# Optimization experiments

Measured on AMD Instinct MI355X. Metric: run time of the kernel, lower is better.

## Reference

```python
import jax, jax.numpy as jnp
import numpy as np

B, G, A, C = 128, 16, 8732, 21
THR = 0.5        # overlap_threshold
NEG_POS = 3      # neg_pos_ratio
VAR0, VAR1 = 0.1, 0.2  # loc_variance


def center_to_point(b):
    cxcy, wh = b[:, :2], b[:, 2:]
    return jnp.concatenate([cxcy - wh / 2, cxcy + wh / 2], axis=-1)


def iou_matrix(a, b):
    # a: [G,4], b: [A,4] point coords (x1,y1,x2,y2) -> [G,A]
    tl = jnp.maximum(a[:, None, :2], b[None, :, :2])
    br = jnp.minimum(a[:, None, 2:], b[None, :, 2:])
    wh = jnp.clip(br - tl, 0.0)
    inter = wh[..., 0] * wh[..., 1]
    area_a = (a[:, 2] - a[:, 0]) * (a[:, 3] - a[:, 1])
    area_b = (b[:, 2] - b[:, 0]) * (b[:, 3] - b[:, 1])
    return inter / (area_a[:, None] + area_b[None, :] - inter)


def encode(anchors, gt_pt):
    # anchors [A,4] (cx,cy,w,h); gt_pt [A,4] point coords
    g_cxcy = (gt_pt[:, :2] + gt_pt[:, 2:]) / 2
    g_wh = gt_pt[:, 2:] - gt_pt[:, :2]
    d_cxcy = (g_cxcy - anchors[:, :2]) / (anchors[:, 2:] * VAR0)
    d_wh = jnp.log(g_wh / anchors[:, 2:]) / VAR1
    return jnp.concatenate([d_cxcy, d_wh], axis=-1)


def match(boxes, labels, anchors, anchors_pt):
    # boxes [G,4] point coords, labels [G] int
    iou = iou_matrix(boxes, anchors_pt)           # [G,A]
    anchor_index = jnp.argmax(iou, axis=1)        # best anchor per gt, [G]
    gt_overlap = jnp.max(iou, axis=0)             # best gt overlap per anchor, [A]
    gt_index = jnp.argmax(iou, axis=0)            # best gt per anchor, [A]
    gt_overlap = gt_overlap.at[anchor_index].set(1.0)
    for i in range(G):
        gt_index = gt_index.at[anchor_index[i]].set(i)
    gt_coords = boxes[gt_index]                   # [A,4]
    loc = encode(anchors, gt_coords)              # [A,4]
    conf = labels[gt_index] + 1                   # [A], 0 reserved for background
    conf = jnp.where(gt_overlap < THR, 0, conf)
    return loc, conf


def setup_inputs() -> dict:
    key = jax.random.key(0)
    k1, k2, k3, k4, k5, k6, k7 = jax.random.split(key, 7)
    predict_offset_coords = jax.random.normal(k1, (B, A, 4), jnp.float32)
    predict_confidences = jax.random.normal(k2, (B, A, C), jnp.float32)
    # valid gt boxes: centers in [0.2,0.8], sizes in [0.05,0.3]
    c = jax.random.uniform(k3, (B, G, 2)) * 0.6 + 0.2
    s = jax.random.uniform(k4, (B, G, 2)) * 0.25 + 0.05
    target_boxes = jnp.concatenate([c - s / 2, c + s / 2], axis=-1)
    target_labels = jax.random.randint(k5, (B, G), 0, C - 1).astype(jnp.int32)
    # anchors in center-coord form (cx,cy,w,h), strictly positive w,h
    acx = jax.random.uniform(k6, (A, 2)) * 0.9 + 0.05
    awh = jax.random.uniform(k7, (A, 2)) * 0.25 + 0.05
    anchors = jnp.concatenate([acx, awh], axis=-1)
    return {"predict_offset_coords": predict_offset_coords,
            "predict_confidences": predict_confidences,
            "target_boxes": target_boxes,
            "target_labels": target_labels,
            "anchors": anchors}


def reference(predict_offset_coords, predict_confidences, target_boxes, target_labels, anchors):
    anchors_pt = center_to_point(anchors)
    loc_t, conf_t = jax.vmap(match, in_axes=(0, 0, None, None))(
        target_boxes, target_labels, anchors, anchors_pt)
    # labels are built without grad in the original (fresh tensors)
    loc_t = jax.lax.stop_gradient(loc_t)
    conf_t = jax.lax.stop_gradient(conf_t)

    is_pos = conf_t > 0                            # [B,A]
    # smooth L1 (beta=1), summed over positive anchors
    diff = predict_offset_coords - loc_t
    ad = jnp.abs(diff)
    sl1 = jnp.where(ad < 1.0, 0.5 * diff * diff, ad - 0.5)
    loss_loc = jnp.sum(sl1 * is_pos[..., None])

    num_pos = jnp.sum(is_pos, axis=1, keepdims=True)      # [B,1]
    n_total = jnp.sum(num_pos).astype(jnp.float32)
    num_neg = jnp.minimum(NEG_POS * num_pos, A - 1)        # [B,1]

    logp = jax.nn.log_softmax(predict_confidences, axis=-1)
    nll = -jnp.take_along_axis(logp, conf_t[..., None], axis=-1)[..., 0]  # [B,A]

    # hard-negative mining via double argsort
    aux = jnp.where(is_pos, 0.0, nll)
    order = jnp.argsort(-aux, axis=1)
    rank = jnp.argsort(order, axis=1)
    is_neg = rank < num_neg

    sel = jnp.logical_or(is_pos, is_neg)
    loss_cls = jnp.sum(jnp.where(sel, nll, 0.0))
    return loss_loc / n_total, loss_cls / n_total
```

## Files before the change

### kernel.cpp

```cpp
#include <hip/hip_runtime.h>
#include <math.h>

#define B_ 128
#define G_ 16
#define A_ 8732
#define C_ 21
#define THR_ 0.5f
#define NEG_POS_ 3
#define VAR0_ 0.1f
#define VAR1_ 0.2f

#define CHUNK_  512
#define NCHUNK_ ((A_ + CHUNK_ - 1) / CHUNK_)
#define TAILA_  (A_ - (NCHUNK_ - 1) * CHUNK_)
#define FULLV_  (CHUNK_ * C_ / 4)
#define TAILV_  (TAILA_ * C_ / 4)
#define NPT_    NCHUNK_

__global__ __launch_bounds__(512) void k_fused(
    const float* __restrict__ pred_off,
    const float* __restrict__ pred_conf,
    const float* __restrict__ tboxes,
    const int*   __restrict__ tlabels,
    const float* __restrict__ anchors,
    float*       __restrict__ lloc_b,
    float*       __restrict__ lcls_b,
    int*         __restrict__ npos_b)
{
    const int b    = blockIdx.x;
    const int tid  = threadIdx.x;
    const int lane = tid & 63;
    const int w    = tid >> 6;

    __shared__ float         s_ov[A_];
    __shared__ unsigned char s_gi[A_];
    __shared__ float         s_aux[A_];
    __shared__ float4        s_stage[FULLV_];
    __shared__ float s_boxlds[G_ * 4];
    __shared__ int   s_lab[G_];
    __shared__ unsigned long long s_gb[8 * G_];
    __shared__ int   s_forced[G_];
    __shared__ int   s_cnt[8];
    __shared__ int   s_c[2][8];
    __shared__ float s_r0[8], s_r1[8], s_r3[8];
    __shared__ int   s_r2[8];

    if (tid < G_ * 4) s_boxlds[tid] = tboxes[b * G_ * 4 + tid];
    if (tid < G_)     s_lab[tid]    = tlabels[b * G_ + tid];
    __syncthreads();

    float bx0[G_], by0[G_], bx1[G_], by1[G_], bar[G_];
    #pragma unroll
    for (int g = 0; g < G_; ++g) {
        bx0[g] = s_boxlds[g * 4 + 0];
        by0[g] = s_boxlds[g * 4 + 1];
        bx1[g] = s_boxlds[g * 4 + 2];
        by1[g] = s_boxlds[g * 4 + 3];
        bar[g] = (bx1[g] - bx0[g]) * (by1[g] - by0[g]);
    }

    unsigned long long gb[G_];
    #pragma unroll
    for (int g = 0; g < G_; ++g) gb[g] = 0ull;

    for (int a = tid; a < A_; a += 512) {
        float4 an = ((const float4*)anchors)[a];
        float ax0 = an.x - an.z * 0.5f, ay0 = an.y - an.w * 0.5f;
        float ax1 = an.x + an.z * 0.5f, ay1 = an.y + an.w * 0.5f;
        float area_b = (ax1 - ax0) * (ay1 - ay0);
        float bov = -1.f; int bg = 0;
        #pragma unroll
        for (int g = 0; g < G_; ++g) {
            float tlx = fmaxf(bx0[g], ax0);
            float tly = fmaxf(by0[g], ay0);
            float brx = fminf(bx1[g], ax1);
            float bry = fminf(by1[g], ay1);
            float wdt = fmaxf(brx - tlx, 0.f);
            float hgt = fmaxf(bry - tly, 0.f);
            float inter = wdt * hgt;
            float iou = inter / (bar[g] + area_b - inter);
            if (iou > bov) { bov = iou; bg = g; }
            unsigned long long pk =
                ((unsigned long long)__float_as_uint(iou) << 32) |
                (unsigned)(~(unsigned)a);
            if (pk > gb[g]) gb[g] = pk;
        }
        s_ov[a] = bov;
        s_gi[a] = (unsigned char)bg;
    }

    #pragma unroll
    for (int g = 0; g < G_; ++g) {
        #pragma unroll
        for (int off = 32; off > 0; off >>= 1) {
            unsigned long long o = __shfl_down(gb[g], off);
            if (o > gb[g]) gb[g] = o;
        }
    }
    if (lane == 0) {
        #pragma unroll
        for (int g = 0; g < G_; ++g) s_gb[w * G_ + g] = gb[g];
    }
    __syncthreads();
    if (tid < G_) {
        unsigned long long m = 0ull;
        #pragma unroll
        for (int wv = 0; wv < 8; ++wv) {
            unsigned long long v = s_gb[wv * G_ + tid];
            if (v > m) m = v;
        }
        s_forced[tid] = (int)(~(unsigned)(m & 0xFFFFFFFFull));
    }
    __syncthreads();
    if (tid == 0) {
        for (int g = 0; g < G_; ++g) {
            int a = s_forced[g];
            s_ov[a] = 1.0f;
            s_gi[a] = (unsigned char)g;
        }
    }

    float lloc = 0.f, pnll = 0.f;
    int   cnt  = 0;

    for (int cc = 0; cc < NCHUNK_; ++cc) {
        const int nv = (cc == NCHUNK_ - 1) ? TAILV_ : FULLV_;
        __syncthreads();
        const float4* g4 = (const float4*)pred_conf
                         + ((((size_t)b * A_) + (size_t)cc * CHUNK_) * C_ >> 2);
        for (int idx = tid; idx < nv; idx += 512) s_stage[idx] = g4[idx];
        __syncthreads();

        const int a = cc * CHUNK_ + tid;
        float auxv = 0.f;
        if (a < A_) {
            const float* sc = (const float*)s_stage + tid * C_;
            float m = sc[0];
            #pragma unroll
            for (int c = 1; c < C_; ++c) m = fmaxf(m, sc[c]);
            float s = 0.f;
            #pragma unroll
            for (int c = 0; c < C_; ++c) s += __expf(sc[c] - m);
            float lse = m + __logf(s);

            float ov  = s_ov[a];
            int   g   = s_gi[a];
            int  conf = (ov < THR_) ? 0 : (s_lab[g] + 1);
            float xc  = sc[conf];
            float nll = lse - xc;
            bool  pos = conf > 0;
            auxv = pos ? 0.f : nll;

            if (pos) {
                cnt++;
                pnll += nll;
                float4 an = ((const float4*)anchors)[a];
                float bxx0 = s_boxlds[g * 4 + 0], bxy0 = s_boxlds[g * 4 + 1];
                float bxx1 = s_boxlds[g * 4 + 2], bxy1 = s_boxlds[g * 4 + 3];
                float gcx = (bxx0 + bxx1) * 0.5f, gcy = (bxy0 + bxy1) * 0.5f;
                float gw = bxx1 - bxx0, gh = bxy1 - bxy0;
                float l0 = (gcx - an.x) / (an.z * VAR0_);
                float l1 = (gcy - an.y) / (an.w * VAR0_);
                float l2 = logf(gw / an.z) / VAR1_;
                float l3 = logf(gh / an.w) / VAR1_;
                float4 p = ((const float4*)pred_off)[(size_t)b * A_ + a];
                float d, ad;
                d = p.x - l0; ad = fabsf(d); lloc += (ad < 1.f) ? 0.5f * d * d : ad - 0.5f;
                d = p.y - l1; ad = fabsf(d); lloc += (ad < 1.f) ? 0.5f * d * d : ad - 0.5f;
                d = p.z - l2; ad = fabsf(d); lloc += (ad < 1.f) ? 0.5f * d * d : ad - 0.5f;
                d = p.w - l3; ad = fabsf(d); lloc += (ad < 1.f) ? 0.5f * d * d : ad - 0.5f;
            }
        }
        if (a < A_) s_aux[a] = auxv;
    }

    {
        int c = cnt;
        #pragma unroll
        for (int off = 32; off > 0; off >>= 1) c += __shfl_down(c, off);
        if (lane == 0) s_cnt[w] = c;
    }
    __syncthreads();
    int npos = 0;
    #pragma unroll
    for (int wv = 0; wv < 8; ++wv) npos += s_cnt[wv];
    if (tid == 0) npos_b[b] = npos;
    const int K = min(NEG_POS_ * npos, A_ - 1);

    unsigned u[NPT_];
    #pragma unroll
    for (int j = 0; j < NPT_; ++j) {
        int a = tid + j * 512;
        u[j] = (a < A_) ? __float_as_uint(s_aux[a]) : 0u;
    }

    unsigned lo = 0u, hi = 0x7f800000u;
    int it = 0;
    while (lo < hi) {
        unsigned mid = (lo + hi) >> 1;
        int c = 0;
        #pragma unroll
        for (int j = 0; j < NPT_; ++j) c += (u[j] > mid);
        #pragma unroll
        for (int off = 32; off > 0; off >>= 1) c += __shfl_down(c, off);
        if (lane == 0) s_c[it & 1][w] = c;
        __syncthreads();
        int total = 0;
        #pragma unroll
        for (int wv = 0; wv < 8; ++wv) total += s_c[it & 1][wv];
        if (total >= K) lo = mid + 1; else hi = mid;
        ++it;
    }

    int selc = 0; float selsm = 0.f;
    #pragma unroll
    for (int j = 0; j < NPT_; ++j) {
        if (u[j] > lo) { selc++; selsm += __uint_as_float(u[j]); }
    }

    #pragma unroll
    for (int off = 32; off > 0; off >>= 1) {
        lloc  += __shfl_down(lloc, off);
        pnll  += __shfl_down(pnll, off);
        selc  += __shfl_down(selc, off);
        selsm += __shfl_down(selsm, off);
    }
    if (lane == 0) { s_r0[w] = lloc; s_r1[w] = pnll; s_r2[w] = selc; s_r3[w] = selsm; }
    __syncthreads();
    if (tid == 0) {
        float L = 0.f, P = 0.f, S = 0.f; int Cc = 0;
        #pragma unroll
        for (int wv = 0; wv < 8; ++wv) {
            L += s_r0[wv]; P += s_r1[wv]; Cc += s_r2[wv]; S += s_r3[wv];
        }
        float T = __uint_as_float(lo);
        lloc_b[b] = L;
        lcls_b[b] = P + S + (float)(K - Cc) * T;
    }
}

__global__ __launch_bounds__(128) void k_fin(
    const float* __restrict__ lloc_b,
    const float* __restrict__ lcls_b,
    const int*   __restrict__ npos_b,
    float*       __restrict__ out)
{
    const int tid  = threadIdx.x;
    const int lane = tid & 63;
    const int w    = tid >> 6;
    __shared__ float s_l[2], s_c[2];
    __shared__ int   s_n[2];

    float L = lloc_b[tid];
    float Cc = lcls_b[tid];
    int   n = npos_b[tid];
    #pragma unroll
    for (int off = 32; off > 0; off >>= 1) {
        L  += __shfl_down(L, off);
        Cc += __shfl_down(Cc, off);
        n  += __shfl_down(n, off);
    }
    if (lane == 0) { s_l[w] = L; s_c[w] = Cc; s_n[w] = n; }
    __syncthreads();
    if (tid == 0) {
        float ntot = (float)(s_n[0] + s_n[1]);
        out[0] = (s_l[0] + s_l[1]) / ntot;
        out[1] = (s_c[0] + s_c[1]) / ntot;
    }
}

extern "C" void kernel_launch(void* const* d_in, const int* in_sizes, int n_in,
                              void* d_out, int out_size, void* d_ws, size_t ws_size,
                              hipStream_t stream) {
    const float* pred_off  = (const float*)d_in[0];
    const float* pred_conf = (const float*)d_in[1];
    const float* tboxes    = (const float*)d_in[2];
    const int*   tlabels   = (const int*)  d_in[3];
    const float* anchors   = (const float*)d_in[4];
    float* out = (float*)d_out;

    char* ws = (char*)d_ws;
    float* lloc_ws = (float*)ws;  ws += (size_t)B_ * sizeof(float);
    float* lcls_ws = (float*)ws;  ws += (size_t)B_ * sizeof(float);
    int*   npos_ws = (int*)ws;

    k_fused<<<B_, 512, 0, stream>>>(pred_off, pred_conf, tboxes, tlabels, anchors,
                                    lloc_ws, lcls_ws, npos_ws);
    k_fin<<<1, 128, 0, stream>>>(lloc_ws, lcls_ws, npos_ws, out);
}
```

Before: 265.8 us.

## Split matching into separate kernel and double-buffer conf staging via async LDS loads

Splits the fused kernel into a matching kernel that writes packed conf/gt-index per anchor plus positive counts, and a loss/selection kernel. The loss kernel double-buffers pred_conf chunks in LDS using global_load_lds direct-to-LDS loads, prefetching the next chunk while the current one is computed. This aims to hide global load latency and cut LDS pressure, which may raise occupancy. The cost is an extra kernel launch and a B*A int round-trip through global memory, with only 128 blocks.

```diff
diff --git a/kernel.cpp b/kernel.cpp
--- a/kernel.cpp
+++ b/kernel.cpp
@@ -10,6 +10,7 @@
 #define VAR0_ 0.1f
 #define VAR1_ 0.2f
 
+#define BA_     (B_ * A_)
 #define CHUNK_  512
 #define NCHUNK_ ((A_ + CHUNK_ - 1) / CHUNK_)
 #define TAILA_  (A_ - (NCHUNK_ - 1) * CHUNK_)
@@ -17,15 +18,19 @@
 #define TAILV_  (TAILA_ * C_ / 4)
 #define NPT_    NCHUNK_
 
-__global__ __launch_bounds__(512) void k_fused(
-    const float* __restrict__ pred_off,
-    const float* __restrict__ pred_conf,
+__device__ __forceinline__ void stage16(const float4* g, float4* l) {
+    __builtin_amdgcn_global_load_lds(
+        (const __attribute__((address_space(1))) void*)g,
+        (__attribute__((address_space(3))) void*)l,
+        16, 0, 0);
+}
+
+__global__ __launch_bounds__(512) void k_match(
     const float* __restrict__ tboxes,
     const int*   __restrict__ tlabels,
     const float* __restrict__ anchors,
-    float*       __restrict__ lloc_b,
-    float*       __restrict__ lcls_b,
-    int*         __restrict__ npos_b)
+    int*         __restrict__ match,
+    int*         __restrict__ num_pos)
 {
     const int b    = blockIdx.x;
     const int tid  = threadIdx.x;
@@ -34,16 +39,11 @@
 
     __shared__ float         s_ov[A_];
     __shared__ unsigned char s_gi[A_];
-    __shared__ float         s_aux[A_];
-    __shared__ float4        s_stage[FULLV_];
     __shared__ float s_boxlds[G_ * 4];
     __shared__ int   s_lab[G_];
     __shared__ unsigned long long s_gb[8 * G_];
     __shared__ int   s_forced[G_];
     __shared__ int   s_cnt[8];
-    __shared__ int   s_c[2][8];
-    __shared__ float s_r0[8], s_r1[8], s_r3[8];
-    __shared__ int   s_r2[8];
 
     if (tid < G_ * 4) s_boxlds[tid] = tboxes[b * G_ * 4 + tid];
     if (tid < G_)     s_lab[tid]    = tlabels[b * G_ + tid];
@@ -119,22 +119,83 @@
             s_gi[a] = (unsigned char)g;
         }
     }
+    __syncthreads();
+
+    int cnt = 0;
+    for (int a = tid; a < A_; a += 512) {
+        float ov = s_ov[a];
+        int g = s_gi[a];
+        int conf = (ov < THR_) ? 0 : (s_lab[g] + 1);
+        match[b * A_ + a] = conf | (g << 8);
+        cnt += (conf > 0);
+    }
+    #pragma unroll
+    for (int off = 32; off > 0; off >>= 1) cnt += __shfl_down(cnt, off);
+    if (lane == 0) s_cnt[w] = cnt;
+    __syncthreads();
+    if (tid == 0) {
+        int t = 0;
+        #pragma unroll
+        for (int wv = 0; wv < 8; ++wv) t += s_cnt[wv];
+        num_pos[b] = t;
+    }
+}
+
+__global__ __launch_bounds__(512) void k_loss_sel(
+    const float* __restrict__ pred_off,
+    const float* __restrict__ pred_conf,
+    const float* __restrict__ tboxes,
+    const float* __restrict__ anchors,
+    const int*   __restrict__ match,
+    const int*   __restrict__ num_pos,
+    float*       __restrict__ lloc_b,
+    float*       __restrict__ lcls_b)
+{
+    const int b    = blockIdx.x;
+    const int tid  = threadIdx.x;
+    const int lane = tid & 63;
+    const int w    = tid >> 6;
+
+    __shared__ float4 s_stage[2][FULLV_];
+    __shared__ float  s_aux[A_];
+    __shared__ int    s_c[2][8];
+    __shared__ float  s_r0[8], s_r1[8], s_r3[8];
+    __shared__ int    s_r2[8];
 
     float lloc = 0.f, pnll = 0.f;
-    int   cnt  = 0;
+    const float4* gb4 = (const float4*)pred_conf + (size_t)b * (A_ * C_ / 4);
+
+    #pragma unroll
+    for (int j = 0; j < 6; ++j) {
+        int idx = tid + j * 512;
+        if (idx < FULLV_) stage16(gb4 + idx, &s_stage[0][idx]);
+    }
+    int mkcur = match[(size_t)b * A_ + tid];
+    __syncthreads();
 
     for (int cc = 0; cc < NCHUNK_; ++cc) {
-        const int nv = (cc == NCHUNK_ - 1) ? TAILV_ : FULLV_;
-        __syncthreads();
-        const float4* g4 = (const float4*)pred_conf
-                         + ((((size_t)b * A_) + (size_t)cc * CHUNK_) * C_ >> 2);
-        for (int idx = tid; idx < nv; idx += 512) s_stage[idx] = g4[idx];
-        __syncthreads();
+        const int cur = cc & 1;
+        const int nxt = cc + 1;
+        int mknext = 0;
+        if (nxt < NCHUNK_) {
+            if (nxt < NCHUNK_ - 1) {
+                const float4* src = gb4 + (size_t)nxt * FULLV_;
+                #pragma unroll
+                for (int j = 0; j < 6; ++j) {
+                    int idx = tid + j * 512;
+                    if (idx < FULLV_) stage16(src + idx, &s_stage[cur ^ 1][idx]);
+                }
+            } else {
+                const float4* src = gb4 + (size_t)nxt * FULLV_;
+                if (tid < TAILV_) s_stage[cur ^ 1][tid] = src[tid];
+            }
+            int an = nxt * CHUNK_ + tid;
+            if (an < A_) mknext = match[(size_t)b * A_ + an];
+        }
 
         const int a = cc * CHUNK_ + tid;
-        float auxv = 0.f;
         if (a < A_) {
-            const float* sc = (const float*)s_stage + tid * C_;
+            const float* sc = (const float*)&s_stage[cur][0] + tid * C_;
             float m = sc[0];
             #pragma unroll
             for (int c = 1; c < C_; ++c) m = fmaxf(m, sc[c]);
@@ -143,26 +204,23 @@
             for (int c = 0; c < C_; ++c) s += __expf(sc[c] - m);
             float lse = m + __logf(s);
 
-            float ov  = s_ov[a];
-            int   g   = s_gi[a];
-            int  conf = (ov < THR_) ? 0 : (s_lab[g] + 1);
+            int conf = mkcur & 0xff;
+            int g    = mkcur >> 8;
             float xc  = sc[conf];
             float nll = lse - xc;
             bool  pos = conf > 0;
-            auxv = pos ? 0.f : nll;
+            s_aux[a] = pos ? 0.f : nll;
 
             if (pos) {
-                cnt++;
                 pnll += nll;
-                float4 an = ((const float4*)anchors)[a];
-                float bxx0 = s_boxlds[g * 4 + 0], bxy0 = s_boxlds[g * 4 + 1];
-                float bxx1 = s_boxlds[g * 4 + 2], bxy1 = s_boxlds[g * 4 + 3];
-                float gcx = (bxx0 + bxx1) * 0.5f, gcy = (bxy0 + bxy1) * 0.5f;
-                float gw = bxx1 - bxx0, gh = bxy1 - bxy0;
-                float l0 = (gcx - an.x) / (an.z * VAR0_);
-                float l1 = (gcy - an.y) / (an.w * VAR0_);
-                float l2 = logf(gw / an.z) / VAR1_;
-                float l3 = logf(gh / an.w) / VAR1_;
+                float4 an4 = ((const float4*)anchors)[a];
+                float4 bx  = ((const float4*)tboxes)[b * G_ + g];
+                float gcx = (bx.x + bx.z) * 0.5f, gcy = (bx.y + bx.w) * 0.5f;
+                float gw = bx.z - bx.x, gh = bx.w - bx.y;
+                float l0 = (gcx - an4.x) / (an4.z * VAR0_);
+                float l1 = (gcy - an4.y) / (an4.w * VAR0_);
+                float l2 = logf(gw / an4.z) / VAR1_;
+                float l3 = logf(gh / an4.w) / VAR1_;
                 float4 p = ((const float4*)pred_off)[(size_t)b * A_ + a];
                 float d, ad;
                 d = p.x - l0; ad = fabsf(d); lloc += (ad < 1.f) ? 0.5f * d * d : ad - 0.5f;
@@ -171,21 +229,10 @@
                 d = p.w - l3; ad = fabsf(d); lloc += (ad < 1.f) ? 0.5f * d * d : ad - 0.5f;
             }
         }
-        if (a < A_) s_aux[a] = auxv;
-    }
-
-    {
-        int c = cnt;
-        #pragma unroll
-        for (int off = 32; off > 0; off >>= 1) c += __shfl_down(c, off);
-        if (lane == 0) s_cnt[w] = c;
-    }
-    __syncthreads();
-    int npos = 0;
-    #pragma unroll
-    for (int wv = 0; wv < 8; ++wv) npos += s_cnt[wv];
-    if (tid == 0) npos_b[b] = npos;
-    const int K = min(NEG_POS_ * npos, A_ - 1);
+
+        __syncthreads();
+        mkcur = mknext;
+    }
 
     unsigned u[NPT_];
     #pragma unroll
@@ -193,6 +240,9 @@
         int a = tid + j * 512;
         u[j] = (a < A_) ? __float_as_uint(s_aux[a]) : 0u;
     }
+
+    const int npos = num_pos[b];
+    const int K = min(NEG_POS_ * npos, A_ - 1);
 
     unsigned lo = 0u, hi = 0x7f800000u;
     int it = 0;
@@ -280,11 +330,13 @@
     float* out = (float*)d_out;
 
     char* ws = (char*)d_ws;
-    float* lloc_ws = (float*)ws;  ws += (size_t)B_ * sizeof(float);
-    float* lcls_ws = (float*)ws;  ws += (size_t)B_ * sizeof(float);
-    int*   npos_ws = (int*)ws;
-
-    k_fused<<<B_, 512, 0, stream>>>(pred_off, pred_conf, tboxes, tlabels, anchors,
-                                    lloc_ws, lcls_ws, npos_ws);
+    int*   match_ws = (int*)ws;   ws += (size_t)BA_ * sizeof(int);
+    float* lloc_ws  = (float*)ws; ws += (size_t)B_ * sizeof(float);
+    float* lcls_ws  = (float*)ws; ws += (size_t)B_ * sizeof(float);
+    int*   npos_ws  = (int*)ws;
+
+    k_match<<<B_, 512, 0, stream>>>(tboxes, tlabels, anchors, match_ws, npos_ws);
+    k_loss_sel<<<B_, 512, 0, stream>>>(pred_off, pred_conf, tboxes, anchors,
+                                       match_ws, npos_ws, lloc_ws, lcls_ws);
     k_fin<<<1, 128, 0, stream>>>(lloc_ws, lcls_ws, npos_ws, out);
 }
```

Result: faster. 239.1 us (-10.1%).
